# Optimization experiments

Measured on AMD Instinct MI355X. Metric: run time of the kernel, lower is better.

Reference implementation:

```python
import jax, jax.numpy as jnp
import numpy as np

N_NODES = 100000
D = 128
N_EDGES = 1600000
N_LAYERS = 3


def setup_inputs() -> dict:
    key = jax.random.key(0)
    k1, k2, k3, k4 = jax.random.split(key, 4)
    emb = jax.random.normal(k1, (N_NODES, D), dtype=jnp.float32)
    vals = jax.random.uniform(k2, (N_EDGES,), dtype=jnp.float32)
    rows = jax.random.randint(k3, (N_EDGES,), 0, N_NODES, dtype=jnp.int64 if jax.config.jax_enable_x64 else jnp.int32)
    cols = jax.random.randint(k4, (N_EDGES,), 0, N_NODES, dtype=jnp.int64 if jax.config.jax_enable_x64 else jnp.int32)
    return {"emb": emb, "vals": vals, "rows": rows, "cols": cols}


def _spmm(vals, rows, cols, x, n):
    # sparse COO matmul: out[r] += v * x[c]
    gathered = vals[:, None] * x[cols]          # [E, D]
    return jax.ops.segment_sum(gathered, rows, num_segments=n)


def reference(emb, vals, rows, cols):
    # Eval path (no edge dropout). NOTE: source never reassigns users_emb
    # inside the layer loop, so every layer computes A @ E0. Faithful output:
    # mean over [E0, A@E0, A@E0, ..., A@E0] (N_LAYERS copies of side).
    n = emb.shape[0]
    side = _spmm(vals, rows, cols, emb, n)      # [N, D], identical each layer
    light_out = (emb + N_LAYERS * side) / (N_LAYERS + 1)
    return light_out
```

## Files before the change

### kernel.cpp

```cpp
#include <hip/hip_runtime.h>
#include <hip/hip_fp16.h>

#define D 128
#define BSHIFT 7
#define NR (1 << BSHIFT)
#define NBMAX 1024

#define P1_TPB 256
#define P1_EPT 16
#define P1_CHUNK (P1_TPB * P1_EPT)
#define CONV_BLOCKS 1024

#define GB_TPB 512
#define GB_CAP 3072

typedef float v4f __attribute__((ext_vector_type(4)));


__global__ __launch_bounds__(P1_TPB) void p1_conv_fc(
        const float* __restrict__ vals, const int* __restrict__ rows,
        const int* __restrict__ cols, int* __restrict__ bucket_fill,
        unsigned* __restrict__ edges, int n_edges, int nb, int p1_blocks,
        const float* __restrict__ emb, __half* __restrict__ emb_h, int n4) {
    int t = threadIdx.x;
    if ((int)blockIdx.x >= p1_blocks) {
        int cb = blockIdx.x - p1_blocks;
        int i = cb * P1_TPB + t;
        int stride = CONV_BLOCKS * P1_TPB;
        const v4f* e4 = reinterpret_cast<const v4f*>(emb);
        uint2* h4 = reinterpret_cast<uint2*>(emb_h);
        for (; i < n4; i += stride) {
            v4f v = __builtin_nontemporal_load(e4 + i);
            __half2 a = __floats2half2_rn(v.x, v.y);
            __half2 b = __floats2half2_rn(v.z, v.w);
            uint2 o;
            o.x = *reinterpret_cast<unsigned*>(&a);
            o.y = *reinterpret_cast<unsigned*>(&b);
            h4[i] = o;
        }
        return;
    }
    __shared__ int cnt[NBMAX];
    __shared__ int sbase[NBMAX];
    __shared__ int gbase[NBMAX];
    __shared__ int scanbuf[P1_TPB];
    __shared__ unsigned stg[P1_CHUNK];
    __shared__ unsigned short stb[P1_CHUNK];

    int base = blockIdx.x * P1_CHUNK;
    int nvalid = n_edges - base;
    if (nvalid <= 0) return;
    if (nvalid > P1_CHUNK) nvalid = P1_CHUNK;

    for (int b = t; b < NBMAX; b += P1_TPB) cnt[b] = 0;
    __syncthreads();

    int bk[P1_EPT], rk[P1_EPT];
    unsigned rc[P1_EPT];
#pragma unroll
    for (int j = 0; j < P1_EPT; ++j) {
        int i = t + j * P1_TPB;
        if (i < nvalid) {
            int e = base + i;
            int r = __builtin_nontemporal_load(rows + e);
            int c = __builtin_nontemporal_load(cols + e);
            float v = __builtin_nontemporal_load(vals + e);
            bk[j] = r >> BSHIFT;
            unsigned vq = (unsigned)(v * 255.f + 0.5f);
            rc[j] = (unsigned)c | ((unsigned)(r & (NR - 1)) << 17) | (vq << 24);
            rk[j] = atomicAdd(&cnt[bk[j]], 1);
        } else {
            bk[j] = -1;
        }
    }
    __syncthreads();

    int c4[4];
    int s = 0;
#pragma unroll
    for (int k = 0; k < 4; ++k) {
        c4[k] = cnt[t * 4 + k];
        s += c4[k];
    }
    scanbuf[t] = s;
    __syncthreads();
    for (int off = 1; off < P1_TPB; off <<= 1) {
        int v = (t >= off) ? scanbuf[t - off] : 0;
        __syncthreads();
        scanbuf[t] += v;
        __syncthreads();
    }
    int run = scanbuf[t] - s;
#pragma unroll
    for (int k = 0; k < 4; ++k) {
        sbase[t * 4 + k] = run;
        run += c4[k];
    }
    __syncthreads();

#pragma unroll
    for (int j = 0; j < P1_EPT; ++j) {
        if (bk[j] >= 0) {
            int slot = sbase[bk[j]] + rk[j];
            stg[slot] = rc[j];
            stb[slot] = (unsigned short)bk[j];
        }
    }
    for (int b = t; b < nb; b += P1_TPB) {
        int c = cnt[b];
        if (c) gbase[b] = atomicAdd(&bucket_fill[b], c);
    }
    __syncthreads();

    for (int i = t; i < nvalid; i += P1_TPB) {
        int b = stb[i];
        int pos = gbase[b] + (i - sbase[b]);
        if (pos < GB_CAP) {
            edges[(size_t)b * GB_CAP + pos] = stg[i];
        }
    }
}

__global__ __launch_bounds__(GB_TPB) void gather_fc(
        const __half* __restrict__ emb_h, const unsigned* __restrict__ edges,
        const int* __restrict__ bucket_fill, float* __restrict__ out,
        int n_rows) {
    __shared__ unsigned stage_c[GB_CAP];
    __shared__ unsigned short order_[GB_CAP];
    __shared__ int rcnt[NR];
    __shared__ int rlo[NR];
    __shared__ int rhi[NR];
    __shared__ int rcur[NR];
    __shared__ int tmp[NR];

    int t = threadIdx.x;
    int b = blockIdx.x;
    int rbase = b << BSHIFT;
    int nr = n_rows - rbase;
    if (nr > NR) nr = NR;
    if (nr <= 0) return;

    int cnt = bucket_fill[b];
    if (cnt > GB_CAP) cnt = GB_CAP;
    if (cnt < 0) cnt = 0;

    if (t < NR) rcnt[t] = 0;
    __syncthreads();

    const unsigned* ep = edges + (size_t)b * GB_CAP;
    for (int i = t; i < cnt; i += GB_TPB) {
        unsigned rec = __builtin_nontemporal_load(ep + i);
        stage_c[i] = rec;
        atomicAdd(&rcnt[(rec >> 17) & (NR - 1)], 1);
    }
    __syncthreads();

    int c0 = (t < NR) ? rcnt[t] : 0;
    int v = c0;
    for (int off = 1; off < NR; off <<= 1) {
        if (t < NR) tmp[t] = v;
        __syncthreads();
        if (t < NR && t >= off) v += tmp[t - off];
        __syncthreads();
    }
    if (t < NR) { rlo[t] = v - c0; rcur[t] = v - c0; rhi[t] = v; }
    __syncthreads();

    for (int i = t; i < cnt; i += GB_TPB) {
        int lr = (stage_c[i] >> 17) & (NR - 1);
        order_[atomicAdd(&rcur[lr], 1)] = (unsigned short)i;
    }
    __syncthreads();

    int w = t >> 6;
    int lane = t & 63;
    int quarter = lane >> 4;
    int sub = lane & 15;
    const uint4* eh4 = reinterpret_cast<const uint4*>(emb_h);
    const float inv = 0.75f / 255.f;

    for (int lr = w; lr < nr; lr += (GB_TPB >> 6)) {
        int row = rbase + lr;
        int eb = rlo[lr];
        int ee = rhi[lr];
        v4f accA = {0.f, 0.f, 0.f, 0.f};
        v4f accB = {0.f, 0.f, 0.f, 0.f};

        int e = eb;
        for (; e + 7 < ee; e += 8) {
            unsigned a0 = stage_c[order_[e + quarter]];
            unsigned a1 = stage_c[order_[e + 4 + quarter]];
            uint4 h0 = eh4[(size_t)(a0 & 0x1FFFFu) * 16 + sub];
            uint4 h1 = eh4[(size_t)(a1 & 0x1FFFFu) * 16 + sub];
            float s0 = (float)(a0 >> 24) * inv;
            float s1 = (float)(a1 >> 24) * inv;
            float2 p;
            p = __half22float2(*reinterpret_cast<const __half2*>(&h0.x));
            accA.x += s0 * p.x; accA.y += s0 * p.y;
            p = __half22float2(*reinterpret_cast<const __half2*>(&h0.y));
            accA.z += s0 * p.x; accA.w += s0 * p.y;
            p = __half22float2(*reinterpret_cast<const __half2*>(&h0.z));
            accB.x += s0 * p.x; accB.y += s0 * p.y;
            p = __half22float2(*reinterpret_cast<const __half2*>(&h0.w));
            accB.z += s0 * p.x; accB.w += s0 * p.y;
            p = __half22float2(*reinterpret_cast<const __half2*>(&h1.x));
            accA.x += s1 * p.x; accA.y += s1 * p.y;
            p = __half22float2(*reinterpret_cast<const __half2*>(&h1.y));
            accA.z += s1 * p.x; accA.w += s1 * p.y;
            p = __half22float2(*reinterpret_cast<const __half2*>(&h1.z));
            accB.x += s1 * p.x; accB.y += s1 * p.y;
            p = __half22float2(*reinterpret_cast<const __half2*>(&h1.w));
            accB.z += s1 * p.x; accB.w += s1 * p.y;
        }
        for (; e < ee; e += 4) {
            int idx = e + quarter;
            bool valid = idx < ee;
            unsigned a = stage_c[order_[valid ? idx : e]];
            uint4 h = eh4[(size_t)(a & 0x1FFFFu) * 16 + sub];
            float s = valid ? (float)(a >> 24) * inv : 0.0f;
            float2 p;
            p = __half22float2(*reinterpret_cast<const __half2*>(&h.x));
            accA.x += s * p.x; accA.y += s * p.y;
            p = __half22float2(*reinterpret_cast<const __half2*>(&h.y));
            accA.z += s * p.x; accA.w += s * p.y;
            p = __half22float2(*reinterpret_cast<const __half2*>(&h.z));
            accB.x += s * p.x; accB.y += s * p.y;
            p = __half22float2(*reinterpret_cast<const __half2*>(&h.w));
            accB.z += s * p.x; accB.w += s * p.y;
        }

        accA.x += __shfl_xor(accA.x, 16); accA.x += __shfl_xor(accA.x, 32);
        accA.y += __shfl_xor(accA.y, 16); accA.y += __shfl_xor(accA.y, 32);
        accA.z += __shfl_xor(accA.z, 16); accA.z += __shfl_xor(accA.z, 32);
        accA.w += __shfl_xor(accA.w, 16); accA.w += __shfl_xor(accA.w, 32);
        accB.x += __shfl_xor(accB.x, 16); accB.x += __shfl_xor(accB.x, 32);
        accB.y += __shfl_xor(accB.y, 16); accB.y += __shfl_xor(accB.y, 32);
        accB.z += __shfl_xor(accB.z, 16); accB.z += __shfl_xor(accB.z, 32);
        accB.w += __shfl_xor(accB.w, 16); accB.w += __shfl_xor(accB.w, 32);

        if (quarter == 0) {
            uint4 hb = eh4[(size_t)row * 16 + sub];
            float2 p;
            p = __half22float2(*reinterpret_cast<const __half2*>(&hb.x));
            accA.x += 0.25f * p.x; accA.y += 0.25f * p.y;
            p = __half22float2(*reinterpret_cast<const __half2*>(&hb.y));
            accA.z += 0.25f * p.x; accA.w += 0.25f * p.y;
            p = __half22float2(*reinterpret_cast<const __half2*>(&hb.z));
            accB.x += 0.25f * p.x; accB.y += 0.25f * p.y;
            p = __half22float2(*reinterpret_cast<const __half2*>(&hb.w));
            accB.z += 0.25f * p.x; accB.w += 0.25f * p.y;
            v4f* o4 = reinterpret_cast<v4f*>(out) + (size_t)row * 32 + sub * 2;
            __builtin_nontemporal_store(accA, o4);
            __builtin_nontemporal_store(accB, o4 + 1);
        }
    }
}

__global__ void lightgcn_init(const float* __restrict__ emb,
                              float* __restrict__ out, int n4) {
    int i = blockIdx.x * blockDim.x + threadIdx.x;
    int stride = gridDim.x * blockDim.x;
    const float4* e4 = reinterpret_cast<const float4*>(emb);
    float4* o4 = reinterpret_cast<float4*>(out);
    for (; i < n4; i += stride) {
        float4 v = e4[i];
        o4[i] = make_float4(0.25f * v.x, 0.25f * v.y, 0.25f * v.z, 0.25f * v.w);
    }
}

__global__ void lightgcn_spmm(const float* __restrict__ emb,
                              const float* __restrict__ vals,
                              const int* __restrict__ rows,
                              const int* __restrict__ cols,
                              float* __restrict__ out, int n_edges) {
    int gtid = blockIdx.x * blockDim.x + threadIdx.x;
    int wave = gtid >> 6;
    int lane = threadIdx.x & 63;
    int n_waves = (gridDim.x * blockDim.x) >> 6;
    for (int e = wave; e < n_edges; e += n_waves) {
        float scale = 0.75f * vals[e];
        int r = rows[e];
        int c = cols[e];
        float2 src = reinterpret_cast<const float2*>(emb + (size_t)c * D)[lane];
        float* dst = out + (size_t)r * D + 2 * lane;
        atomicAdd(dst + 0, scale * src.x);
        atomicAdd(dst + 1, scale * src.y);
    }
}

extern "C" void kernel_launch(void* const* d_in, const int* in_sizes, int n_in,
                              void* d_out, int out_size, void* d_ws, size_t ws_size,
                              hipStream_t stream) {
    const float* emb  = (const float*)d_in[0];
    const float* vals = (const float*)d_in[1];
    const int*   rows = (const int*)d_in[2];
    const int*   cols = (const int*)d_in[3];
    float* out = (float*)d_out;

    int n_edges = in_sizes[1];
    int n_rows  = out_size / D;
    int nb = (n_rows + NR - 1) >> BSHIFT;
    int n4 = n_rows * D / 4;

    size_t emb_h_bytes = (size_t)n_rows * D * 2;
    size_t slab_bytes  = (size_t)nb * GB_CAP * 4;
    size_t needA = slab_bytes + emb_h_bytes + (size_t)nb * 4;

    bool okShape = (nb <= NBMAX) && (n_rows < (1 << 17));
    int p1_blocks = (n_edges + P1_CHUNK - 1) / P1_CHUNK;

    if (okShape && ws_size >= needA + 256) {
        char* p = (char*)d_ws;
        unsigned* edges = (unsigned*)p;  p += slab_bytes;
        __half*   embh  = (__half*)p;    p += emb_h_bytes;
        int* bucket_fill = (int*)p;

        hipMemsetAsync(bucket_fill, 0, (size_t)nb * 4, stream);
        p1_conv_fc<<<p1_blocks + CONV_BLOCKS, P1_TPB, 0, stream>>>(
            vals, rows, cols, bucket_fill, edges, n_edges, nb, p1_blocks,
            emb, embh, n4);
        gather_fc<<<nb, GB_TPB, 0, stream>>>(embh, edges, bucket_fill,
                                             out, n_rows);
        return;
    }

    int nq = out_size / 4;
    lightgcn_init<<<2048, 256, 0, stream>>>(emb, out, nq);
    lightgcn_spmm<<<8192, 256, 0, stream>>>(emb, vals, rows, cols, out, n_edges);
}
```

Before: 111.6 us.

## Split wavefront into two 32-lane halves with 8-byte gathers per lane

Reworks the per-row gather so each wavefront handles two edges at a time, with 32 lanes per edge each loading 8 bytes of the fp16 row, instead of four edges with 16 lanes loading 16 bytes. Four independent gathers are issued per lane per iteration, the accumulators shrink to a single float4, and the cross-lane reduction drops to one shuffle stage. The aim is more memory-level parallelism per lane and fewer registers, traded against narrower loads. It also halves the per-thread edge count in the partition pass (P1_EPT 16 to 8), which launches more blocks there.

```diff
diff --git a/kernel.cpp b/kernel.cpp
--- a/kernel.cpp
+++ b/kernel.cpp
@@ -7,7 +7,7 @@
 #define NBMAX 1024
 
 #define P1_TPB 256
-#define P1_EPT 16
+#define P1_EPT 8
 #define P1_CHUNK (P1_TPB * P1_EPT)
 #define CONV_BLOCKS 1024
 
@@ -174,84 +174,78 @@
 
     int w = t >> 6;
     int lane = t & 63;
-    int quarter = lane >> 4;
-    int sub = lane & 15;
-    const uint4* eh4 = reinterpret_cast<const uint4*>(emb_h);
+    int half = lane >> 5;
+    int sub = lane & 31;
+    const uint2* eh = reinterpret_cast<const uint2*>(emb_h);
     const float inv = 0.75f / 255.f;
 
     for (int lr = w; lr < nr; lr += (GB_TPB >> 6)) {
         int row = rbase + lr;
         int eb = rlo[lr];
         int ee = rhi[lr];
-        v4f accA = {0.f, 0.f, 0.f, 0.f};
-        v4f accB = {0.f, 0.f, 0.f, 0.f};
+        float4 acc = make_float4(0.f, 0.f, 0.f, 0.f);
 
         int e = eb;
         for (; e + 7 < ee; e += 8) {
-            unsigned a0 = stage_c[order_[e + quarter]];
-            unsigned a1 = stage_c[order_[e + 4 + quarter]];
-            uint4 h0 = eh4[(size_t)(a0 & 0x1FFFFu) * 16 + sub];
-            uint4 h1 = eh4[(size_t)(a1 & 0x1FFFFu) * 16 + sub];
+            unsigned a0 = stage_c[order_[e + 0 + half]];
+            unsigned a1 = stage_c[order_[e + 2 + half]];
+            unsigned a2 = stage_c[order_[e + 4 + half]];
+            unsigned a3 = stage_c[order_[e + 6 + half]];
+            uint2 h0 = eh[(size_t)(a0 & 0x1FFFFu) * 32 + sub];
+            uint2 h1 = eh[(size_t)(a1 & 0x1FFFFu) * 32 + sub];
+            uint2 h2 = eh[(size_t)(a2 & 0x1FFFFu) * 32 + sub];
+            uint2 h3 = eh[(size_t)(a3 & 0x1FFFFu) * 32 + sub];
             float s0 = (float)(a0 >> 24) * inv;
             float s1 = (float)(a1 >> 24) * inv;
-            float2 p;
+            float s2 = (float)(a2 >> 24) * inv;
+            float s3 = (float)(a3 >> 24) * inv;
+            float2 p, q;
             p = __half22float2(*reinterpret_cast<const __half2*>(&h0.x));
-            accA.x += s0 * p.x; accA.y += s0 * p.y;
-            p = __half22float2(*reinterpret_cast<const __half2*>(&h0.y));
-            accA.z += s0 * p.x; accA.w += s0 * p.y;
-            p = __half22float2(*reinterpret_cast<const __half2*>(&h0.z));
-            accB.x += s0 * p.x; accB.y += s0 * p.y;
-            p = __half22float2(*reinterpret_cast<const __half2*>(&h0.w));
-            accB.z += s0 * p.x; accB.w += s0 * p.y;
+            q = __half22float2(*reinterpret_cast<const __half2*>(&h0.y));
+            acc.x += s0 * p.x; acc.y += s0 * p.y; acc.z += s0 * q.x; acc.w += s0 * q.y;
             p = __half22float2(*reinterpret_cast<const __half2*>(&h1.x));
-            accA.x += s1 * p.x; accA.y += s1 * p.y;
-            p = __half22float2(*reinterpret_cast<const __half2*>(&h1.y));
-            accA.z += s1 * p.x; accA.w += s1 * p.y;
-            p = __half22float2(*reinterpret_cast<const __half2*>(&h1.z));
-            accB.x += s1 * p.x; accB.y += s1 * p.y;
-            p = __half22float2(*reinterpret_cast<const __half2*>(&h1.w));
-            accB.z += s1 * p.x; accB.w += s1 * p.y;
-        }
-        for (; e < ee; e += 4) {
-            int idx = e + quarter;
-            bool valid = idx < ee;
-            unsigned a = stage_c[order_[valid ? idx : e]];
-            uint4 h = eh4[(size_t)(a & 0x1FFFFu) * 16 + sub];
-            float s = valid ? (float)(a >> 24) * inv : 0.0f;
-            float2 p;
-            p = __half22float2(*reinterpret_cast<const __half2*>(&h.x));
-            accA.x += s * p.x; accA.y += s * p.y;
-            p = __half22float2(*reinterpret_cast<const __half2*>(&h.y));
-            accA.z += s * p.x; accA.w += s * p.y;
-            p = __half22float2(*reinterpret_cast<const __half2*>(&h.z));
-            accB.x += s * p.x; accB.y += s * p.y;
-            p = __half22float2(*reinterpret_cast<const __half2*>(&h.w));
-            accB.z += s * p.x; accB.w += s * p.y;
-        }
-
-        accA.x += __shfl_xor(accA.x, 16); accA.x += __shfl_xor(accA.x, 32);
-        accA.y += __shfl_xor(accA.y, 16); accA.y += __shfl_xor(accA.y, 32);
-        accA.z += __shfl_xor(accA.z, 16); accA.z += __shfl_xor(accA.z, 32);
-        accA.w += __shfl_xor(accA.w, 16); accA.w += __shfl_xor(accA.w, 32);
-        accB.x += __shfl_xor(accB.x, 16); accB.x += __shfl_xor(accB.x, 32);
-        accB.y += __shfl_xor(accB.y, 16); accB.y += __shfl_xor(accB.y, 32);
-        accB.z += __shfl_xor(accB.z, 16); accB.z += __shfl_xor(accB.z, 32);
-        accB.w += __shfl_xor(accB.w, 16); accB.w += __shfl_xor(accB.w, 32);
-
-        if (quarter == 0) {
-            uint4 hb = eh4[(size_t)row * 16 + sub];
-            float2 p;
-            p = __half22float2(*reinterpret_cast<const __half2*>(&hb.x));
-            accA.x += 0.25f * p.x; accA.y += 0.25f * p.y;
-            p = __half22float2(*reinterpret_cast<const __half2*>(&hb.y));
-            accA.z += 0.25f * p.x; accA.w += 0.25f * p.y;
-            p = __half22float2(*reinterpret_cast<const __half2*>(&hb.z));
-            accB.x += 0.25f * p.x; accB.y += 0.25f * p.y;
-            p = __half22float2(*reinterpret_cast<const __half2*>(&hb.w));
-            accB.z += 0.25f * p.x; accB.w += 0.25f * p.y;
-            v4f* o4 = reinterpret_cast<v4f*>(out) + (size_t)row * 32 + sub * 2;
-            __builtin_nontemporal_store(accA, o4);
-            __builtin_nontemporal_store(accB, o4 + 1);
+            q = __half22float2(*reinterpret_cast<const __half2*>(&h1.y));
+            acc.x += s1 * p.x; acc.y += s1 * p.y; acc.z += s1 * q.x; acc.w += s1 * q.y;
+            p = __half22float2(*reinterpret_cast<const __half2*>(&h2.x));
+            q = __half22float2(*reinterpret_cast<const __half2*>(&h2.y));
+            acc.x += s2 * p.x; acc.y += s2 * p.y; acc.z += s2 * q.x; acc.w += s2 * q.y;
+            p = __half22float2(*reinterpret_cast<const __half2*>(&h3.x));
+            q = __half22float2(*reinterpret_cast<const __half2*>(&h3.y));
+            acc.x += s3 * p.x; acc.y += s3 * p.y; acc.z += s3 * q.x; acc.w += s3 * q.y;
+        }
+        for (; e + 1 < ee; e += 2) {
+            unsigned a = stage_c[order_[e + half]];
+            uint2 h = eh[(size_t)(a & 0x1FFFFu) * 32 + sub];
+            float s = (float)(a >> 24) * inv;
+            float2 p = __half22float2(*reinterpret_cast<const __half2*>(&h.x));
+            float2 q = __half22float2(*reinterpret_cast<const __half2*>(&h.y));
+            acc.x += s * p.x; acc.y += s * p.y; acc.z += s * q.x; acc.w += s * q.y;
+        }
+        if (e < ee) {
+            unsigned a = stage_c[order_[e]];
+            uint2 h = eh[(size_t)(a & 0x1FFFFu) * 32 + sub];
+            float s = (half == 0) ? (float)(a >> 24) * inv : 0.0f;
+            float2 p = __half22float2(*reinterpret_cast<const __half2*>(&h.x));
+            float2 q = __half22float2(*reinterpret_cast<const __half2*>(&h.y));
+            acc.x += s * p.x; acc.y += s * p.y; acc.z += s * q.x; acc.w += s * q.y;
+        }
+
+        acc.x += __shfl_xor(acc.x, 32);
+        acc.y += __shfl_xor(acc.y, 32);
+        acc.z += __shfl_xor(acc.z, 32);
+        acc.w += __shfl_xor(acc.w, 32);
+
+        if (half == 0) {
+            uint2 hb = eh[(size_t)row * 32 + sub];
+            float2 p = __half22float2(*reinterpret_cast<const __half2*>(&hb.x));
+            float2 q = __half22float2(*reinterpret_cast<const __half2*>(&hb.y));
+            v4f o;
+            o.x = acc.x + 0.25f * p.x;
+            o.y = acc.y + 0.25f * p.y;
+            o.z = acc.z + 0.25f * q.x;
+            o.w = acc.w + 0.25f * q.y;
+            __builtin_nontemporal_store(o,
+                reinterpret_cast<v4f*>(out) + (size_t)row * 32 + sub);
         }
     }
 }
```

After: 123.4 us. +10.6%, slower.
